# Optimization experiments

Hardware: AMD Instinct MI355X
Metric: run time of the kernel (lower is better)

The kernel has to match this reference:

```python
import jax, jax.numpy as jnp
import numpy as np

BZ, SEQ, IN_SZ, HID_SZ = 256, 512, 256, 256


def setup_inputs() -> dict:
    key = jax.random.key(0)
    k1, k2, k3, k4, k5 = jax.random.split(key, 5)
    stdv = 1.0 / np.sqrt(HID_SZ)
    return {
        "encoder_inputs": jax.random.normal(k1, (BZ, HID_SZ), dtype=jnp.float32),
        "decoder_inputs": jax.random.normal(k2, (BZ, SEQ, IN_SZ), dtype=jnp.float32),
        "U_i": jax.random.uniform(k3, (IN_SZ, HID_SZ), minval=-stdv, maxval=stdv, dtype=jnp.float32),
        "V_i": jax.random.uniform(k4, (HID_SZ, HID_SZ), minval=-stdv, maxval=stdv, dtype=jnp.float32),
        "b_i": jax.random.uniform(k5, (HID_SZ,), minval=-stdv, maxval=stdv, dtype=jnp.float32),
    }


def reference(encoder_inputs, decoder_inputs, U_i, V_i, b_i):
    # Sequential vanilla-RNN recurrence over time via lax.scan.
    # h_t = tanh(x_t @ U_i + h_{t-1} @ V_i + b_i)
    xs = jnp.swapaxes(decoder_inputs, 0, 1)  # [seq, bz, in]

    def step(h, x_t):
        h_new = jnp.tanh(x_t @ U_i + h @ V_i + b_i)
        return h_new, h_new

    _, outs = jax.lax.scan(step, encoder_inputs, xs)  # outs: [seq, bz, hid]
    decoder_outputs = jnp.swapaxes(outs, 0, 1)  # [bz, seq, hid]
    return (encoder_inputs, decoder_outputs)
```

## Files before the change

### kernel.cpp

```cpp
#include <hip/hip_runtime.h>
#include <hip/hip_bf16.h>


#define SEQn 512
#define HIDn 256

typedef __attribute__((ext_vector_type(4))) float  floatx4;
typedef __attribute__((ext_vector_type(8))) short  short8;

__device__ __forceinline__ short f2bf(float f) {
    __hip_bfloat16 h = __float2bfloat16(f);
    return *reinterpret_cast<short*>(&h);
}

__global__ void prep_B(const float* __restrict__ U, short* __restrict__ wsB) {
    int idx = blockIdx.x * 256 + threadIdx.x;
    int n  = idx & 255;
    int q  = (idx >> 8) & 3;
    int kb = idx >> 10;
    int k0 = kb * 32 + q * 8;
    short8 c;
    #pragma unroll
    for (int j = 0; j < 8; j++)
        c[j] = f2bf(U[(size_t)(k0 + j) * 256 + n]);
    *(short8*)(wsB + (size_t)idx * 8) = c;
}

__global__ __launch_bounds__(256, 4)
void xu_gemm(const float* __restrict__ X, const short* __restrict__ wsB,
             const float* __restrict__ bias, float* __restrict__ out)
{
    const int tid = threadIdx.x;
    const int l   = tid & 63;
    const int w   = tid >> 6;
    const int lr  = l & 15;
    const int q   = l >> 4;
    const int m0  = blockIdx.y * 128;
    const int n0  = blockIdx.x * 128;

    floatx4 acc[2][8];
    #pragma unroll
    for (int mt = 0; mt < 2; mt++)
        #pragma unroll
        for (int nt = 0; nt < 8; nt++)
            acc[mt][nt] = (floatx4){0.f, 0.f, 0.f, 0.f};

    const size_t rowA = (size_t)(m0 + 32 * w + lr);

    for (int kb = 0; kb < 8; kb++) {
        short8 af[2];
        #pragma unroll
        for (int mt = 0; mt < 2; mt++) {
            const float* p = X + (rowA + 16 * mt) * 256 + kb * 32 + q * 8;
            float4 a0 = *(const float4*)p;
            float4 a1 = *(const float4*)(p + 4);
            af[mt][0] = f2bf(a0.x); af[mt][1] = f2bf(a0.y);
            af[mt][2] = f2bf(a0.z); af[mt][3] = f2bf(a0.w);
            af[mt][4] = f2bf(a1.x); af[mt][5] = f2bf(a1.y);
            af[mt][6] = f2bf(a1.z); af[mt][7] = f2bf(a1.w);
        }
        #pragma unroll
        for (int nt = 0; nt < 8; nt++) {
            short8 bfr = *(const short8*)(wsB +
                ((size_t)(kb * 4 + q) * 256 + n0 + 16 * nt + lr) * 8);
            acc[0][nt] = __builtin_amdgcn_mfma_f32_16x16x32_bf16(af[0], bfr, acc[0][nt], 0, 0, 0);
            acc[1][nt] = __builtin_amdgcn_mfma_f32_16x16x32_bf16(af[1], bfr, acc[1][nt], 0, 0, 0);
        }
    }

    #pragma unroll
    for (int nt = 0; nt < 8; nt++) {
        float bv = bias[n0 + 16 * nt + lr];
        #pragma unroll
        for (int mt = 0; mt < 2; mt++) {
            #pragma unroll
            for (int r = 0; r < 4; r++) {
                int row = m0 + 32 * w + 16 * mt + 4 * q + r;
                out[(size_t)row * 256 + n0 + 16 * nt + lr] = acc[mt][nt][r] + bv;
            }
        }
    }
}

__global__ __launch_bounds__(512, 2)
void rnn_rec(const float* __restrict__ enc, const float* __restrict__ V,
             float* __restrict__ out)
{
    __shared__ float hbuf[HIDn];
    __shared__ float part[8][HIDn];

    const int tid = threadIdx.x;
    const int w   = tid >> 6;
    const int l   = tid & 63;
    const int b   = blockIdx.x;

    float4 v[32];
    #pragma unroll
    for (int kk = 0; kk < 32; kk++)
        v[kk] = *(const float4*)(V + (size_t)(32 * w + kk) * 256 + 4 * l);

    float* outEnc = out + (size_t)b * HIDn;
    float* outDec = out + (size_t)65536 + (size_t)b * SEQn * HIDn;

    if (tid < HIDn) {
        float h0 = enc[(size_t)b * HIDn + tid];
        hbuf[tid]   = h0;
        outEnc[tid] = h0;
    }
    float xu_cur = 0.f;
    if (tid < HIDn) xu_cur = outDec[tid];
    __syncthreads();

    for (int t = 0; t < SEQn; t++) {
        float xu_next = 0.f;
        if (tid < HIDn && t + 1 < SEQn)
            xu_next = outDec[(size_t)(t + 1) * HIDn + tid];

        float hv = hbuf[32 * w + (l & 31)];
        int   hvi = __builtin_bit_cast(int, hv);

        float4 acc = make_float4(0.f, 0.f, 0.f, 0.f);
        #pragma unroll
        for (int kk = 0; kk < 32; kk++) {
            float hs = __builtin_bit_cast(float, __builtin_amdgcn_readlane(hvi, kk));
            float4 vv = v[kk];
            acc.x = fmaf(hs, vv.x, acc.x);
            acc.y = fmaf(hs, vv.y, acc.y);
            acc.z = fmaf(hs, vv.z, acc.z);
            acc.w = fmaf(hs, vv.w, acc.w);
        }
        *(float4*)&part[w][4 * l] = acc;
        __syncthreads();

        if (tid < HIDn) {
            float s = xu_cur;
            #pragma unroll
            for (int ww = 0; ww < 8; ww++) s += part[ww][tid];
            float e = __expf(2.f * s);
            float h = 1.f - 2.f / (e + 1.f);
            hbuf[tid] = h;
            outDec[(size_t)t * HIDn + tid] = h;
        }
        xu_cur = xu_next;
        __syncthreads();
    }
}

extern "C" void kernel_launch(void* const* d_in, const int* in_sizes, int n_in,
                              void* d_out, int out_size, void* d_ws, size_t ws_size,
                              hipStream_t stream) {
    const float* enc  = (const float*)d_in[0];
    const float* x    = (const float*)d_in[1];
    const float* U    = (const float*)d_in[2];
    const float* V    = (const float*)d_in[3];
    const float* bias = (const float*)d_in[4];
    float* out = (float*)d_out;

    float* outDec = out + 65536;

    short* wsB = (ws_size >= 131072) ? (short*)d_ws : (short*)out;

    prep_B<<<32, 256, 0, stream>>>(U, wsB);

    dim3 ggrid(2, 1024);
    xu_gemm<<<ggrid, 256, 0, stream>>>(x, wsB, bias, outDec);

    rnn_rec<<<256, 512, 0, stream>>>(enc, V, out);
}
```

Baseline: 603.5 us.

## Use fp16 MFMA for recurrent h·V with double-buffered hidden state

Replaces the per-step scalar FMA matvec (readlane broadcast plus cross-wave partial-sum reduction through shared memory) with 16x16x32 fp16 MFMA instructions, with V held in registers as fp16 fragments. The hidden state is stored in double-buffered fp16 shared memory, which removes one of the two barriers per timestep. XU prefetch is extended to two steps ahead. Only row 0 of the MFMA output is used, so most of the MFMA work is wasted, and fp16 rounding of h and V lowers accuracy in a 512-step recurrence.

```diff
diff --git a/kernel.cpp b/kernel.cpp
--- a/kernel.cpp
+++ b/kernel.cpp
@@ -5,8 +5,9 @@
 #define SEQn 512
 #define HIDn 256
 
-typedef __attribute__((ext_vector_type(4))) float  floatx4;
-typedef __attribute__((ext_vector_type(8))) short  short8;
+typedef __attribute__((ext_vector_type(4))) float    floatx4;
+typedef __attribute__((ext_vector_type(8))) short    short8;
+typedef __attribute__((ext_vector_type(8))) _Float16 half8;
 
 __device__ __forceinline__ short f2bf(float f) {
     __hip_bfloat16 h = __float2bfloat16(f);
@@ -86,62 +87,90 @@
 void rnn_rec(const float* __restrict__ enc, const float* __restrict__ V,
              float* __restrict__ out)
 {
-    __shared__ float hbuf[HIDn];
-    __shared__ float part[8][HIDn];
+    __shared__ _Float16 hbuf[2][HIDn];
 
     const int tid = threadIdx.x;
     const int w   = tid >> 6;
     const int l   = tid & 63;
+    const int lr  = l & 15;
+    const int q   = l >> 4;
     const int b   = blockIdx.x;
+    const int c0  = 32 * w + lr;
 
-    float4 v[32];
+    half8 vf[2][8];
     #pragma unroll
-    for (int kk = 0; kk < 32; kk++)
-        v[kk] = *(const float4*)(V + (size_t)(32 * w + kk) * 256 + 4 * l);
+    for (int c = 0; c < 8; c++) {
+        const float* vp = V + (size_t)(32 * c + 8 * q) * HIDn + 32 * w + lr;
+        #pragma unroll
+        for (int nt = 0; nt < 2; nt++) {
+            half8 tmp;
+            #pragma unroll
+            for (int j = 0; j < 8; j++)
+                tmp[j] = (_Float16)vp[(size_t)j * HIDn + 16 * nt];
+            vf[nt][c] = tmp;
+        }
+    }
 
     float* outEnc = out + (size_t)b * HIDn;
     float* outDec = out + (size_t)65536 + (size_t)b * SEQn * HIDn;
 
     if (tid < HIDn) {
         float h0 = enc[(size_t)b * HIDn + tid];
-        hbuf[tid]   = h0;
-        outEnc[tid] = h0;
+        outEnc[tid]  = h0;
+        hbuf[0][tid] = (_Float16)h0;
     }
-    float xu_cur = 0.f;
-    if (tid < HIDn) xu_cur = outDec[tid];
+
+    float xu_cur0 = outDec[c0];
+    float xu_cur1 = outDec[c0 + 16];
+    float xu_nx0  = outDec[HIDn + c0];
+    float xu_nx1  = outDec[HIDn + c0 + 16];
+
     __syncthreads();
 
+    int p = 0;
     for (int t = 0; t < SEQn; t++) {
-        float xu_next = 0.f;
-        if (tid < HIDn && t + 1 < SEQn)
-            xu_next = outDec[(size_t)(t + 1) * HIDn + tid];
+        float pf0 = 0.f, pf1 = 0.f;
+        if (t + 2 < SEQn) {
+            const float* xp = outDec + (size_t)(t + 2) * HIDn;
+            pf0 = xp[c0];
+            pf1 = xp[c0 + 16];
+        }
 
-        float hv = hbuf[32 * w + (l & 31)];
-        int   hvi = __builtin_bit_cast(int, hv);
+        half8 af[8];
+        #pragma unroll
+        for (int c = 0; c < 8; c++)
+            af[c] = *(const half8*)&hbuf[p][32 * c + 8 * q];
 
-        float4 acc = make_float4(0.f, 0.f, 0.f, 0.f);
+        floatx4 a0a = (floatx4){0.f,0.f,0.f,0.f};
+        floatx4 a0b = (floatx4){0.f,0.f,0.f,0.f};
+        floatx4 a1a = (floatx4){0.f,0.f,0.f,0.f};
+        floatx4 a1b = (floatx4){0.f,0.f,0.f,0.f};
         #pragma unroll
-        for (int kk = 0; kk < 32; kk++) {
-            float hs = __builtin_bit_cast(float, __builtin_amdgcn_readlane(hvi, kk));
-            float4 vv = v[kk];
-            acc.x = fmaf(hs, vv.x, acc.x);
-            acc.y = fmaf(hs, vv.y, acc.y);
-            acc.z = fmaf(hs, vv.z, acc.z);
-            acc.w = fmaf(hs, vv.w, acc.w);
+        for (int c = 0; c < 8; c += 2) {
+            a0a = __builtin_amdgcn_mfma_f32_16x16x32_f16(af[c],     vf[0][c],     a0a, 0, 0, 0);
+            a1a = __builtin_amdgcn_mfma_f32_16x16x32_f16(af[c],     vf[1][c],     a1a, 0, 0, 0);
+            a0b = __builtin_amdgcn_mfma_f32_16x16x32_f16(af[c + 1], vf[0][c + 1], a0b, 0, 0, 0);
+            a1b = __builtin_amdgcn_mfma_f32_16x16x32_f16(af[c + 1], vf[1][c + 1], a1b, 0, 0, 0);
         }
-        *(float4*)&part[w][4 * l] = acc;
-        __syncthreads();
 
-        if (tid < HIDn) {
-            float s = xu_cur;
-            #pragma unroll
-            for (int ww = 0; ww < 8; ww++) s += part[ww][tid];
-            float e = __expf(2.f * s);
-            float h = 1.f - 2.f / (e + 1.f);
-            hbuf[tid] = h;
-            outDec[(size_t)t * HIDn + tid] = h;
+        float s0 = (a0a[0] + a0b[0]) + xu_cur0;
+        float s1 = (a1a[0] + a1b[0]) + xu_cur1;
+        float e0 = __expf(2.f * s0);
+        float e1 = __expf(2.f * s1);
+        float hv0 = 1.f - 2.f / (e0 + 1.f);
+        float hv1 = 1.f - 2.f / (e1 + 1.f);
+
+        if (q == 0) {
+            float* op = outDec + (size_t)t * HIDn;
+            op[c0]      = hv0;
+            op[c0 + 16] = hv1;
+            hbuf[p ^ 1][c0]      = (_Float16)hv0;
+            hbuf[p ^ 1][c0 + 16] = (_Float16)hv1;
         }
-        xu_cur = xu_next;
+
+        xu_cur0 = xu_nx0; xu_cur1 = xu_nx1;
+        xu_nx0  = pf0;    xu_nx1  = pf1;
+        p ^= 1;
         __syncthreads();
     }
 }
```

Result: faster. 572.1 us (-5.2%).
